# Kernel tuning notes

Measured on AMD Instinct MI355X. Metric: run time of the kernel, lower is better.

The kernel has to match this reference:

```python
import jax, jax.numpy as jnp
import numpy as np

B, T, F, L = 512, 512, 128, 512  # batch, seq_len, n_features, latent_dim


def setup_inputs() -> dict:
    key = jax.random.key(0)
    ks = jax.random.split(key, 8)
    s = 1.0 / np.sqrt(L)  # torch default init scale for GRUCell (hidden_size=L)
    sd = 1.0 / np.sqrt(L)  # torch Linear(L, F) init scale
    return {
        "x": jax.random.normal(ks[0], (B, T, F), jnp.float32),
        "h_0": jax.random.normal(ks[1], (1, B, L), jnp.float32),
        "W_ih": jax.random.uniform(ks[2], (3 * L, F), jnp.float32, -s, s),
        "W_hh": jax.random.uniform(ks[3], (3 * L, L), jnp.float32, -s, s),
        "b_ih": jax.random.uniform(ks[4], (3 * L,), jnp.float32, -s, s),
        "b_hh": jax.random.uniform(ks[5], (3 * L,), jnp.float32, -s, s),
        "Wd": jax.random.uniform(ks[6], (F, L), jnp.float32, -sd, sd),
        "bd": jax.random.uniform(ks[7], (F,), jnp.float32, -sd, sd),
        "seq_len": T,
    }


def reference(x, h_0, W_ih, W_hh, b_ih, b_hh, Wd, bd, seq_len):
    # epsilon=0.0 default: teacher forcing never fires, so x_t = dense(h_t).
    h = jnp.squeeze(h_0, axis=0)          # [B, L]
    xt = h @ Wd.T + bd                    # [B, F]  (initial dense(h_0))

    def step(carry, _):
        h, xt = carry
        gi = xt @ W_ih.T + b_ih           # [B, 3L]
        gh = h @ W_hh.T + b_hh            # [B, 3L]
        i_r, i_z, i_n = jnp.split(gi, 3, axis=-1)
        h_r, h_z, h_n = jnp.split(gh, 3, axis=-1)
        r = jax.nn.sigmoid(i_r + h_r)
        z = jax.nn.sigmoid(i_z + h_z)
        n = jnp.tanh(i_n + r * h_n)
        h_new = (1.0 - z) * n + z * h     # [B, L]
        x_new = h_new @ Wd.T + bd         # [B, F] == dense(h_t) == output[:, t]
        return (h_new, x_new), x_new

    _, ys = jax.lax.scan(step, (h, xt), None, length=seq_len)  # ys: [T, B, F]
    return jnp.transpose(ys, (1, 0, 2))   # [B, T, F]
```

## Files before the change

### kernel.cpp

```cpp
#include <hip/hip_runtime.h>
#include <stdint.h>

typedef _Float16 f16;
typedef _Float16 half8 __attribute__((ext_vector_type(8)));
typedef _Float16 half4 __attribute__((ext_vector_type(4)));
typedef float float4v __attribute__((ext_vector_type(4)));
typedef float float2v __attribute__((ext_vector_type(2)));
typedef unsigned int u32;

#define MFMA16(A, B, C) __builtin_amdgcn_mfma_f32_16x16x32_f16((A), (B), (C), 0, 0, 0)

static constexpr int Bsz = 512, Tsz = 512, Fsz = 128, Lsz = 512;
static constexpr int NPACK = 2176;
static constexpr float LO_S = 2048.0f, LO_R = 1.0f / 2048.0f;

static constexpr size_t WSZ_FRAG  = (size_t)(NPACK / 16) * 16 * 64 * 8 * 2;
static constexpr size_t OFF_WHI   = 0;
static constexpr size_t OFF_WLO   = OFF_WHI + WSZ_FRAG;
static constexpr size_t OFF_BIAS  = OFF_WLO + WSZ_FRAG;
static constexpr size_t OFF_HX    = OFF_BIAS + 16384;
static constexpr size_t OFF_FLAGS = OFF_HX + (size_t)2 * 1024 * 1024;


static constexpr int LDS_H  = 0;
static constexpr int EXS = 37;
static constexpr int LDS_EX = 65536;
static constexpr int LDS_YP = LDS_EX + 16 * 32 * EXS * 4;
static constexpr int LDS_TOT = LDS_YP + 4 * 32 * 17 * 4;

__device__ __forceinline__ void async16(const void* g, void* l) {
  __builtin_amdgcn_global_load_lds((const __attribute__((address_space(1))) u32*)g,
                                   (__attribute__((address_space(3))) u32*)l, 16, 0, 16);
}

__device__ __forceinline__ float sigm(float x) { return 1.0f / (1.0f + __expf(-x)); }
__device__ __forceinline__ float tanh_(float x) { return 1.0f - 2.0f / (__expf(2.0f * x) + 1.0f); }

__global__ void k_pack(const float* __restrict__ Wih, const float* __restrict__ Whh,
                       const float* __restrict__ Wd, f16* __restrict__ whiF,
                       f16* __restrict__ wloF) {
  const int c = blockIdx.y;
  const int l = blockIdx.x * 256 + threadIdx.x;
  float v;
  if (c < 1536) {
    const float* wih = Wih + c * 128;
    float acc = 0.f;
#pragma unroll 8
    for (int f = 0; f < 128; ++f) acc = fmaf(Wd[f * 512 + l], wih[f], acc);
    v = acc;
    if (c < 1024) v += Whh[c * 512 + l];
  } else if (c < 2048) {
    v = Whh[(c - 512) * 512 + l];
  } else {
    v = Wd[(c - 2048) * 512 + l];
  }
  f16 hi = (f16)v;
  f16 lo = (f16)((v - (float)hi) * LO_S);
  const int chunk = c >> 4, ks = l >> 5, q = (l >> 3) & 3, j = l & 7, n = c & 15;
  const size_t idx = (((size_t)(chunk * 16 + ks)) * 64 + q * 16 + n) * 8 + j;
  whiF[idx] = hi;
  wloF[idx] = lo;
}

__global__ void k_init(const float* __restrict__ h0, const float* __restrict__ Wih,
                       const float* __restrict__ bih, const float* __restrict__ bhh,
                       const float* __restrict__ bd, f16* __restrict__ hx,
                       float* __restrict__ biasP, int* __restrict__ flags) {
  const int t = blockIdx.x * 256 + threadIdx.x;
  if (t < Bsz * Lsz) {
    const int row = t >> 9, col = t & 511;
    float v = h0[t];
    f16 hi = (f16)v;
    f16 lo = (f16)((v - (float)hi) * LO_S);
    const int g = row >> 5, rl = row & 31, mt = rl >> 4, n = rl & 15;
    const int mm = col >> 5, cs = col & 31, qq = (cs >> 3) ^ (n & 3), j = cs & 7;
    const size_t b = (size_t)g * 65536 + (size_t)mm * 4096 + mt * 2048 + n * 128 + qq * 32;
    char* p = (char*)hx + b;
    *(f16*)(p + j * 2) = hi;
    *(f16*)(p + 16 + j * 2) = lo;
  }
  if (t < NPACK) {
    float v;
    if (t < 1536) {
      float a = bih[t];
      for (int f = 0; f < 128; ++f) a = fmaf(Wih[t * 128 + f], bd[f], a);
      if (t < 1024) a += bhh[t];
      v = a;
    } else if (t < 2048) {
      v = bhh[t - 512];
    } else {
      v = bd[t - 2048];
    }
    biasP[t] = v;
  }
  if (t < 8192) flags[t] = 0;
}

__global__ __launch_bounds__(256, 1) void k_main(
    const float* __restrict__ h0, const f16* __restrict__ whiF,
    const f16* __restrict__ wloF, const float* __restrict__ biasP,
    f16* __restrict__ hx, int* __restrict__ flags, float* __restrict__ out) {
  extern __shared__ char dsm[];
  float* ex = (float*)(dsm + LDS_EX);
  float* yp = (float*)(dsm + LDS_YP);

  const int bid = blockIdx.x;
  const int g = bid & 15;
  const int m = bid >> 4;
  const int tid = threadIdx.x;
  const int v = tid >> 6, lane = tid & 63, q = lane >> 4, n = lane & 15;

  const half8* whiV = (const half8*)whiF;
  const half8* wloV = (const half8*)wloF;
  half8 w_hi[4][2][4], w_lo[4][2][4];
#pragma unroll
  for (int t = 0; t < 4; ++t)
#pragma unroll
    for (int nt = 0; nt < 2; ++nt)
#pragma unroll
      for (int ks = 0; ks < 4; ++ks) {
        const int idx = ((t * 32 + m * 2 + nt) * 16 + v * 4 + ks) * 64 + lane;
        w_hi[t][nt][ks] = whiV[idx];
        w_lo[t][nt][ks] = wloV[idx];
      }
  half8 w_y[4];
  if (m < 8) {
#pragma unroll
    for (int ks = 0; ks < 4; ++ks) w_y[ks] = whiV[((128 + m) * 16 + v * 4 + ks) * 64 + lane];
  }

  const int rl = tid >> 3, c0 = (tid & 7) * 4;
  float bias[4][4];
#pragma unroll
  for (int t = 0; t < 4; ++t)
#pragma unroll
    for (int cc = 0; cc < 4; ++cc) bias[t][cc] = biasP[t * 512 + m * 32 + c0 + cc];
  float hreg[4];
#pragma unroll
  for (int cc = 0; cc < 4; ++cc)
    hreg[cc] = h0[(size_t)(32 * g + rl) * 512 + m * 32 + c0 + cc];
  const int c2 = (tid & 7) * 2;
  float by[2] = {0.f, 0.f};
  if (m < 8) {
    by[0] = biasP[2048 + m * 16 + c2];
    by[1] = biasP[2048 + m * 16 + c2 + 1];
  }

  const int mtP = rl >> 4, nP = rl & 15;
  const size_t recO = (size_t)m * 4096 + mtP * 2048 + nP * 128 +
                      (((c0 >> 3) ^ (nP & 3)) * 32) + (((c0 >> 2) & 1) * 8);
  const int fragB0 = LDS_H + v * 16384 + n * 128 + ((q ^ (n & 3)) * 32);

  int* myflag = flags + (g * 16 + m) * 16;
  const size_t grpB = (size_t)g * 65536;

  for (int s = 1; s <= 513; ++s) {
    {
      const size_t bufB = (size_t)((s - 1) & 1) * 1048576 + grpB;
#pragma unroll
      for (int j = 0; j < 4; ++j) {
        const int* fa = flags + (g * 16 + (4 * v + j)) * 16;
        while (__hip_atomic_load(fa, __ATOMIC_RELAXED, __HIP_MEMORY_SCOPE_AGENT) < s - 1)
          __builtin_amdgcn_s_sleep(1);
        __builtin_amdgcn_sched_barrier(0);
        const char* src = (const char*)hx + bufB + (size_t)(4 * v + j) * 4096 + lane * 16;
        char* dst = dsm + LDS_H + v * 16384 + j * 4096 + lane * 16;
#pragma unroll
        for (int i = 0; i < 4; ++i) async16(src + i * 1024, dst + i * 1024);
      }
    }
    asm volatile("s_waitcnt vmcnt(0)" ::: "memory");
    __builtin_amdgcn_sched_barrier(0);

#pragma unroll
    for (int p = 0; p < 2; ++p) {
      float4v a_hh[2][2][2], a_ll[2][2][2];
#pragma unroll
      for (int ti = 0; ti < 2; ++ti)
#pragma unroll
        for (int nt = 0; nt < 2; ++nt)
#pragma unroll
          for (int mt = 0; mt < 2; ++mt) {
            a_hh[ti][nt][mt] = (float4v){0,0,0,0};
            a_ll[ti][nt][mt] = (float4v){0,0,0,0};
          }
#pragma unroll
      for (int ks = 0; ks < 4; ++ks) {
        half8 ah[2], al[2];
#pragma unroll
        for (int mt = 0; mt < 2; ++mt) {
          const char* fp = dsm + fragB0 + ks * 4096 + mt * 2048;
          ah[mt] = *(const half8*)fp;
          al[mt] = *(const half8*)(fp + 16);
        }
#pragma unroll
        for (int ti = 0; ti < 2; ++ti) {
          const int t = p * 2 + ti;
#pragma unroll
          for (int nt = 0; nt < 2; ++nt)
#pragma unroll
            for (int mt = 0; mt < 2; ++mt) {
              a_hh[ti][nt][mt] = MFMA16(ah[mt], w_hi[t][nt][ks], a_hh[ti][nt][mt]);
              a_ll[ti][nt][mt] = MFMA16(al[mt], w_hi[t][nt][ks], a_ll[ti][nt][mt]);
              a_ll[ti][nt][mt] = MFMA16(ah[mt], w_lo[t][nt][ks], a_ll[ti][nt][mt]);
            }
        }
      }
#pragma unroll
      for (int ti = 0; ti < 2; ++ti) {
        const int t = p * 2 + ti;
#pragma unroll
        for (int nt = 0; nt < 2; ++nt)
#pragma unroll
          for (int mt = 0; mt < 2; ++mt) {
            const int base = ((t * 4 + v) * 32 + nt * 16 + n) * EXS + mt * 16 + q * 4;
            const float4v vv = a_hh[ti][nt][mt] + a_ll[ti][nt][mt] * LO_R;
            *(float2v*)(ex + base) = (float2v){vv[0], vv[1]};
            *(float2v*)(ex + base + 2) = (float2v){vv[2], vv[3]};
          }
      }
    }
    __syncthreads();

    float pre[4][4];
#pragma unroll
    for (int t = 0; t < 4; ++t)
#pragma unroll
      for (int cc = 0; cc < 4; ++cc) {
        float acc = bias[t][cc];
#pragma unroll
        for (int w = 0; w < 4; ++w) acc += ex[((t * 4 + w) * 32 + c0 + cc) * EXS + rl];
        pre[t][cc] = acc;
      }
    const int rg = 32 * g + rl;
    half4 hiv, lov;
#pragma unroll
    for (int cc = 0; cc < 4; ++cc) {
      const float r = sigm(pre[0][cc]);
      const float z = sigm(pre[1][cc]);
      const float nn = tanh_(fmaf(r, pre[3][cc], pre[2][cc]));
      const float hn = fmaf(z, hreg[cc] - nn, nn);
      hreg[cc] = hn;
      const f16 hi = (f16)hn;
      hiv[cc] = hi;
      lov[cc] = (f16)((hn - (float)hi) * LO_S);
    }
    {
      const size_t ob = (size_t)(s & 1) * 1048576 + grpB + recO;
      __hip_atomic_store((uint64_t*)((char*)hx + ob), __builtin_bit_cast(uint64_t, hiv),
                         __ATOMIC_RELAXED, __HIP_MEMORY_SCOPE_AGENT);
      __hip_atomic_store((uint64_t*)((char*)hx + ob + 16), __builtin_bit_cast(uint64_t, lov),
                         __ATOMIC_RELAXED, __HIP_MEMORY_SCOPE_AGENT);
    }
    asm volatile("s_waitcnt vmcnt(0)" ::: "memory");
    __syncthreads();
    if (tid == 0)
      __hip_atomic_store(myflag, s, __ATOMIC_RELAXED, __HIP_MEMORY_SCOPE_AGENT);

    if (m < 8) {
      float4v yac[2] = {(float4v){0,0,0,0}, (float4v){0,0,0,0}};
#pragma unroll
      for (int ks = 0; ks < 4; ++ks) {
#pragma unroll
        for (int mt = 0; mt < 2; ++mt) {
          const half8 ah = *(const half8*)(dsm + fragB0 + ks * 4096 + mt * 2048);
          yac[mt] = MFMA16(ah, w_y[ks], yac[mt]);
        }
      }
#pragma unroll
      for (int mt = 0; mt < 2; ++mt)
#pragma unroll
        for (int e = 0; e < 4; ++e)
          yp[(v * 32 + mt * 16 + q * 4 + e) * 17 + n] = yac[mt][e];
    }
    __syncthreads();

    if (m < 8 && s >= 2) {
#pragma unroll
      for (int cc = 0; cc < 2; ++cc) {
        float yv = by[cc];
#pragma unroll
        for (int w = 0; w < 4; ++w) yv += yp[(w * 32 + rl) * 17 + c2 + cc];
        __builtin_nontemporal_store(
            yv, out + (size_t)rg * (Tsz * Fsz) + (size_t)(s - 2) * Fsz + m * 16 + c2 + cc);
      }
    }
  }
}

extern "C" void kernel_launch(void* const* d_in, const int* in_sizes, int n_in,
                              void* d_out, int out_size, void* d_ws, size_t ws_size,
                              hipStream_t stream) {
  (void)in_sizes; (void)n_in; (void)out_size; (void)ws_size;
  const float* h0  = (const float*)d_in[1];
  const float* Wih = (const float*)d_in[2];
  const float* Whh = (const float*)d_in[3];
  const float* bih = (const float*)d_in[4];
  const float* bhh = (const float*)d_in[5];
  const float* Wd  = (const float*)d_in[6];
  const float* bd  = (const float*)d_in[7];
  float* out = (float*)d_out;
  char* ws = (char*)d_ws;

  f16* whiF    = (f16*)(ws + OFF_WHI);
  f16* wloF    = (f16*)(ws + OFF_WLO);
  float* biasP = (float*)(ws + OFF_BIAS);
  f16* hx      = (f16*)(ws + OFF_HX);
  int* flags   = (int*)(ws + OFF_FLAGS);

  hipFuncSetAttribute((const void*)k_main, hipFuncAttributeMaxDynamicSharedMemorySize,
                      LDS_TOT);
  k_pack<<<dim3(2, NPACK), 256, 0, stream>>>(Wih, Whh, Wd, whiF, wloF);
  k_init<<<1024, 256, 0, stream>>>(h0, Wih, bih, bhh, bd, hx, biasP, flags);
  k_main<<<256, 256, LDS_TOT, stream>>>(h0, whiF, wloF, biasP, hx, flags, out);
}
```

Baseline: 4.806 ms.

## Overlap hx loads with MFMA, spread output projection across all blocks, pack flags

The hx exchange layout is reorganised so that hi and lo halves live in separate 2KB planes without XOR swizzling. Flags are packed contiguously and polled four at a time before any loads are issued. The per-ks vmcnt waits let MFMA work start as soon as each chunk of h arrives in LDS. The output dense projection moves from 8 blocks onto all 16 and is fused into the main MFMA loop, which removes one __syncthreads and a separate pass. In exchange, packed flags may share cache lines and cause contention, and the unswizzled LDS layout may add bank conflicts.

Result: slower. 5.275 ms (+9.7%).

```diff
diff --git a/kernel.cpp b/kernel.cpp
--- a/kernel.cpp
+++ b/kernel.cpp
@@ -26,7 +26,7 @@
 static constexpr int EXS = 37;
 static constexpr int LDS_EX = 65536;
 static constexpr int LDS_YP = LDS_EX + 16 * 32 * EXS * 4;
-static constexpr int LDS_TOT = LDS_YP + 4 * 32 * 17 * 4;
+static constexpr int LDS_TOT = LDS_YP + 4 * 16 * 17 * 4;
 
 __device__ __forceinline__ void async16(const void* g, void* l) {
   __builtin_amdgcn_global_load_lds((const __attribute__((address_space(1))) u32*)g,
@@ -72,12 +72,11 @@
     float v = h0[t];
     f16 hi = (f16)v;
     f16 lo = (f16)((v - (float)hi) * LO_S);
-    const int g = row >> 5, rl = row & 31, mt = rl >> 4, n = rl & 15;
-    const int mm = col >> 5, cs = col & 31, qq = (cs >> 3) ^ (n & 3), j = cs & 7;
-    const size_t b = (size_t)g * 65536 + (size_t)mm * 4096 + mt * 2048 + n * 128 + qq * 32;
-    char* p = (char*)hx + b;
-    *(f16*)(p + j * 2) = hi;
-    *(f16*)(p + 16 + j * 2) = lo;
+    const int g = row >> 5, rl = row & 31, mm = col >> 5, cs = col & 31;
+    const size_t b = (size_t)g * 65536 + (size_t)mm * 4096 + (rl >> 4) * 1024 +
+                     (rl & 15) * 64 + (cs >> 3) * 16 + ((cs >> 2) & 1) * 8 + (cs & 3) * 2;
+    *(f16*)((char*)hx + b) = hi;
+    *(f16*)((char*)hx + b + 2048) = lo;
   }
   if (t < NPACK) {
     float v;
@@ -109,6 +108,7 @@
   const int m = bid >> 4;
   const int tid = threadIdx.x;
   const int v = tid >> 6, lane = tid & 63, q = lane >> 4, n = lane & 15;
+  const int yt = m >> 1, mty = m & 1;
 
   const half8* whiV = (const half8*)whiF;
   const half8* wloV = (const half8*)wloF;
@@ -124,10 +124,9 @@
         w_lo[t][nt][ks] = wloV[idx];
       }
   half8 w_y[4];
-  if (m < 8) {
-#pragma unroll
-    for (int ks = 0; ks < 4; ++ks) w_y[ks] = whiV[((128 + m) * 16 + v * 4 + ks) * 64 + lane];
-  }
+#pragma unroll
+  for (int ks = 0; ks < 4; ++ks)
+    w_y[ks] = whiV[((128 + yt) * 16 + v * 4 + ks) * 64 + lane];
 
   const int rl = tid >> 3, c0 = (tid & 7) * 4;
   float bias[4][4];
@@ -139,85 +138,90 @@
 #pragma unroll
   for (int cc = 0; cc < 4; ++cc)
     hreg[cc] = h0[(size_t)(32 * g + rl) * 512 + m * 32 + c0 + cc];
-  const int c2 = (tid & 7) * 2;
-  float by[2] = {0.f, 0.f};
-  if (m < 8) {
-    by[0] = biasP[2048 + m * 16 + c2];
-    by[1] = biasP[2048 + m * 16 + c2 + 1];
-  }
-
-  const int mtP = rl >> 4, nP = rl & 15;
-  const size_t recO = (size_t)m * 4096 + mtP * 2048 + nP * 128 +
-                      (((c0 >> 3) ^ (nP & 3)) * 32) + (((c0 >> 2) & 1) * 8);
-  const int fragB0 = LDS_H + v * 16384 + n * 128 + ((q ^ (n & 3)) * 32);
-
-  int* myflag = flags + (g * 16 + m) * 16;
+
+  const int r16 = tid >> 4, c16 = tid & 15;
+  const float by0 = biasP[2048 + yt * 16 + c16];
+  const size_t outRowB = (size_t)(32 * g + mty * 16 + r16) * (Tsz * Fsz) + yt * 16 + c16;
+
+  const size_t recHi = (size_t)g * 65536 + (size_t)m * 4096 + (rl >> 4) * 1024 +
+                       (rl & 15) * 64 + (c0 >> 3) * 16 + ((c0 >> 2) & 1) * 8;
+  const int fragB0 = LDS_H + v * 16384 + 1024 * 0 + n * 64 + q * 16;
+
+  int* fb = flags + g * 16;
   const size_t grpB = (size_t)g * 65536;
 
   for (int s = 1; s <= 513; ++s) {
+    asm volatile("s_waitcnt vmcnt(0)" ::: "memory");
+
+    if (s > 1) {
+      int mn;
+      do {
+        const int f0 = __hip_atomic_load(fb + 4 * v + 0, __ATOMIC_RELAXED, __HIP_MEMORY_SCOPE_AGENT);
+        const int f1 = __hip_atomic_load(fb + 4 * v + 1, __ATOMIC_RELAXED, __HIP_MEMORY_SCOPE_AGENT);
+        const int f2 = __hip_atomic_load(fb + 4 * v + 2, __ATOMIC_RELAXED, __HIP_MEMORY_SCOPE_AGENT);
+        const int f3 = __hip_atomic_load(fb + 4 * v + 3, __ATOMIC_RELAXED, __HIP_MEMORY_SCOPE_AGENT);
+        mn = min(min(f0, f1), min(f2, f3));
+        if (mn < s - 1) __builtin_amdgcn_s_sleep(1);
+      } while (mn < s - 1);
+    }
+    __builtin_amdgcn_sched_barrier(0);
+
     {
-      const size_t bufB = (size_t)((s - 1) & 1) * 1048576 + grpB;
-#pragma unroll
-      for (int j = 0; j < 4; ++j) {
-        const int* fa = flags + (g * 16 + (4 * v + j)) * 16;
-        while (__hip_atomic_load(fa, __ATOMIC_RELAXED, __HIP_MEMORY_SCOPE_AGENT) < s - 1)
-          __builtin_amdgcn_s_sleep(1);
-        __builtin_amdgcn_sched_barrier(0);
-        const char* src = (const char*)hx + bufB + (size_t)(4 * v + j) * 4096 + lane * 16;
-        char* dst = dsm + LDS_H + v * 16384 + j * 4096 + lane * 16;
-#pragma unroll
-        for (int i = 0; i < 4; ++i) async16(src + i * 1024, dst + i * 1024);
-      }
-    }
-    asm volatile("s_waitcnt vmcnt(0)" ::: "memory");
-    __builtin_amdgcn_sched_barrier(0);
-
-#pragma unroll
-    for (int p = 0; p < 2; ++p) {
-      float4v a_hh[2][2][2], a_ll[2][2][2];
-#pragma unroll
-      for (int ti = 0; ti < 2; ++ti)
-#pragma unroll
-        for (int nt = 0; nt < 2; ++nt)
-#pragma unroll
-          for (int mt = 0; mt < 2; ++mt) {
-            a_hh[ti][nt][mt] = (float4v){0,0,0,0};
-            a_ll[ti][nt][mt] = (float4v){0,0,0,0};
+      const char* sb = (const char*)hx + (size_t)((s - 1) & 1) * 1048576 + grpB +
+                       (size_t)(4 * v) * 4096 + lane * 16;
+      char* db = dsm + LDS_H + v * 16384 + lane * 16;
+#pragma unroll
+      for (int j = 0; j < 4; ++j)
+#pragma unroll
+        for (int i = 0; i < 4; ++i)
+          async16(sb + j * 4096 + i * 1024, db + j * 4096 + i * 1024);
+    }
+
+    float4v yac = (float4v){0, 0, 0, 0};
+#pragma unroll
+    for (int mt = 0; mt < 2; ++mt) {
+      float4v a_hh[4][2], a_ll[4][2];
+#pragma unroll
+      for (int t = 0; t < 4; ++t)
+#pragma unroll
+        for (int nt = 0; nt < 2; ++nt) {
+          a_hh[t][nt] = (float4v){0, 0, 0, 0};
+          a_ll[t][nt] = (float4v){0, 0, 0, 0};
+        }
+#pragma unroll
+      for (int ks = 0; ks < 4; ++ks) {
+        if (mt == 0) {
+          if (ks == 0)      asm volatile("s_waitcnt vmcnt(12)" ::: "memory");
+          else if (ks == 1) asm volatile("s_waitcnt vmcnt(8)" ::: "memory");
+          else if (ks == 2) asm volatile("s_waitcnt vmcnt(4)" ::: "memory");
+          else              asm volatile("s_waitcnt vmcnt(0)" ::: "memory");
+          __builtin_amdgcn_sched_barrier(0);
+        }
+        const char* fp = dsm + fragB0 + ks * 4096 + mt * 1024;
+        const half8 ah = *(const half8*)fp;
+        const half8 al = *(const half8*)(fp + 2048);
+#pragma unroll
+        for (int t = 0; t < 4; ++t)
+#pragma unroll
+          for (int nt = 0; nt < 2; ++nt) {
+            a_hh[t][nt] = MFMA16(ah, w_hi[t][nt][ks], a_hh[t][nt]);
+            a_ll[t][nt] = MFMA16(al, w_hi[t][nt][ks], a_ll[t][nt]);
+            a_ll[t][nt] = MFMA16(ah, w_lo[t][nt][ks], a_ll[t][nt]);
           }
-#pragma unroll
-      for (int ks = 0; ks < 4; ++ks) {
-        half8 ah[2], al[2];
-#pragma unroll
-        for (int mt = 0; mt < 2; ++mt) {
-          const char* fp = dsm + fragB0 + ks * 4096 + mt * 2048;
-          ah[mt] = *(const half8*)fp;
-          al[mt] = *(const half8*)(fp + 16);
+        if (mt == mty) yac = MFMA16(ah, w_y[ks], yac);
+      }
+#pragma unroll
+      for (int t = 0; t < 4; ++t)
+#pragma unroll
+        for (int nt = 0; nt < 2; ++nt) {
+          const int base = ((t * 4 + v) * 32 + nt * 16 + n) * EXS + mt * 16 + q * 4;
+          const float4v vv = a_hh[t][nt] + a_ll[t][nt] * LO_R;
+          *(float2v*)(ex + base) = (float2v){vv[0], vv[1]};
+          *(float2v*)(ex + base + 2) = (float2v){vv[2], vv[3]};
         }
-#pragma unroll
-        for (int ti = 0; ti < 2; ++ti) {
-          const int t = p * 2 + ti;
-#pragma unroll
-          for (int nt = 0; nt < 2; ++nt)
-#pragma unroll
-            for (int mt = 0; mt < 2; ++mt) {
-              a_hh[ti][nt][mt] = MFMA16(ah[mt], w_hi[t][nt][ks], a_hh[ti][nt][mt]);
-              a_ll[ti][nt][mt] = MFMA16(al[mt], w_hi[t][nt][ks], a_ll[ti][nt][mt]);
-              a_ll[ti][nt][mt] = MFMA16(ah[mt], w_lo[t][nt][ks], a_ll[ti][nt][mt]);
-            }
-        }
-      }
-#pragma unroll
-      for (int ti = 0; ti < 2; ++ti) {
-        const int t = p * 2 + ti;
-#pragma unroll
-        for (int nt = 0; nt < 2; ++nt)
-#pragma unroll
-          for (int mt = 0; mt < 2; ++mt) {
-            const int base = ((t * 4 + v) * 32 + nt * 16 + n) * EXS + mt * 16 + q * 4;
-            const float4v vv = a_hh[ti][nt][mt] + a_ll[ti][nt][mt] * LO_R;
-            *(float2v*)(ex + base) = (float2v){vv[0], vv[1]};
-            *(float2v*)(ex + base + 2) = (float2v){vv[2], vv[3]};
-          }
+      if (mt == mty) {
+#pragma unroll
+        for (int e = 0; e < 4; ++e) yp[(v * 16 + q * 4 + e) * 17 + n] = yac[e];
       }
     }
     __syncthreads();
@@ -232,7 +236,10 @@
         for (int w = 0; w < 4; ++w) acc += ex[((t * 4 + w) * 32 + c0 + cc) * EXS + rl];
         pre[t][cc] = acc;
       }
-    const int rg = 32 * g + rl;
+    float yv = by0;
+#pragma unroll
+    for (int w = 0; w < 4; ++w) yv += yp[(w * 16 + r16) * 17 + c16];
+
     half4 hiv, lov;
 #pragma unroll
     for (int cc = 0; cc < 4; ++cc) {
@@ -246,45 +253,19 @@
       lov[cc] = (f16)((hn - (float)hi) * LO_S);
     }
     {
-      const size_t ob = (size_t)(s & 1) * 1048576 + grpB + recO;
-      __hip_atomic_store((uint64_t*)((char*)hx + ob), __builtin_bit_cast(uint64_t, hiv),
+      char* ph = (char*)hx + (size_t)(s & 1) * 1048576 + recHi;
+      __hip_atomic_store((uint64_t*)ph, __builtin_bit_cast(uint64_t, hiv),
                          __ATOMIC_RELAXED, __HIP_MEMORY_SCOPE_AGENT);
-      __hip_atomic_store((uint64_t*)((char*)hx + ob + 16), __builtin_bit_cast(uint64_t, lov),
+      __hip_atomic_store((uint64_t*)(ph + 2048), __builtin_bit_cast(uint64_t, lov),
                          __ATOMIC_RELAXED, __HIP_MEMORY_SCOPE_AGENT);
     }
     asm volatile("s_waitcnt vmcnt(0)" ::: "memory");
     __syncthreads();
     if (tid == 0)
-      __hip_atomic_store(myflag, s, __ATOMIC_RELAXED, __HIP_MEMORY_SCOPE_AGENT);
-
-    if (m < 8) {
-      float4v yac[2] = {(float4v){0,0,0,0}, (float4v){0,0,0,0}};
-#pragma unroll
-      for (int ks = 0; ks < 4; ++ks) {
-#pragma unroll
-        for (int mt = 0; mt < 2; ++mt) {
-          const half8 ah = *(const half8*)(dsm + fragB0 + ks * 4096 + mt * 2048);
-          yac[mt] = MFMA16(ah, w_y[ks], yac[mt]);
-        }
-      }
-#pragma unroll
-      for (int mt = 0; mt < 2; ++mt)
-#pragma unroll
-        for (int e = 0; e < 4; ++e)
-          yp[(v * 32 + mt * 16 + q * 4 + e) * 17 + n] = yac[mt][e];
-    }
-    __syncthreads();
-
-    if (m < 8 && s >= 2) {
-#pragma unroll
-      for (int cc = 0; cc < 2; ++cc) {
-        float yv = by[cc];
-#pragma unroll
-        for (int w = 0; w < 4; ++w) yv += yp[(w * 32 + rl) * 17 + c2 + cc];
-        __builtin_nontemporal_store(
-            yv, out + (size_t)rg * (Tsz * Fsz) + (size_t)(s - 2) * Fsz + m * 16 + c2 + cc);
-      }
-    }
+      __hip_atomic_store(fb + m, s, __ATOMIC_RELAXED, __HIP_MEMORY_SCOPE_AGENT);
+
+    if (s >= 2)
+      __builtin_nontemporal_store(yv, out + outRowB + (size_t)(s - 2) * Fsz);
   }
 }
 
```
